# Kernel optimization log

Hardware: AMD Instinct MI355X
Metric: run time of the kernel (lower is better)

Reference implementation:

```python
import jax, jax.numpy as jnp
import numpy as np

IN_DIM = 1024
OUT_DIM = 2048
GRID = 5   # kan_config.grid_size
K = 3      # kan_config.spline_order


def b_splines(x, grid, k):
    """Cox-de Boor recursion.
    x: (N, D), grid: (D, G+2k+1) extended knots. Returns (N, D, G+k) basis values."""
    x = x[..., None]              # (N, D, 1)
    g = grid[None, :, :]          # (1, D, M)
    # degree-0 indicator bases
    B = ((x >= g[..., :-1]) & (x < g[..., 1:])).astype(x.dtype)  # (N, D, M-1)
    for p in range(1, k + 1):
        left = (x - g[..., : -(p + 1)]) / (g[..., p:-1] - g[..., : -(p + 1)])
        right = (g[..., p + 1:] - x) / (g[..., p + 1:] - g[..., 1:-p])
        B = left * B[..., :-1] + right * B[..., 1:]
    return B  # (N, D, G+k)


def setup_inputs() -> dict:
    key = jax.random.key(0)
    k1, k2, k3 = jax.random.split(key, 3)
    # inputs kept inside the spline grid range [-1, 1]
    x = jax.random.uniform(k1, (4, 2048, IN_DIM), jnp.float32, -1.0, 1.0)
    # uniform extended grid over [-1, 1] with k extra knots on each side
    h = 2.0 / GRID
    g = jnp.arange(-K, GRID + K + 1, dtype=jnp.float32) * h - 1.0  # (G+2K+1,)
    grid = jnp.broadcast_to(g, (IN_DIM, GRID + 2 * K + 1)).astype(jnp.float32)
    coef = (jax.random.normal(k2, (IN_DIM, OUT_DIM, GRID + K), jnp.float32) * 0.1)
    scale_base = jax.random.normal(k3, (IN_DIM, OUT_DIM), jnp.float32) * 0.1 + (1.0 / np.sqrt(IN_DIM)).astype(np.float32)
    scale_sp = jnp.ones((IN_DIM, OUT_DIM), jnp.float32)
    return {"x": x, "grid": grid, "coef": coef, "scale_base": scale_base, "scale_sp": scale_sp}


def reference(x, grid, coef, scale_base, scale_sp):
    shp = x.shape
    xf = x.reshape(-1, shp[-1])                 # (N, D)
    B = b_splines(xf, grid, K)                  # (N, D, G+K)
    coef_s = coef * scale_sp[:, :, None]        # fold per-edge spline scale into coefficients
    spline = jnp.einsum('ndg,dog->no', B, coef_s)          # (N, O)
    base = jnp.einsum('nd,do->no', jax.nn.silu(xf), scale_base)  # (N, O)
    out = base + spline
    return out.reshape(shp[:-1] + (OUT_DIM,))
```

## Files before the change

kernel.cpp:

```cpp
#include <hip/hip_runtime.h>
#include <hip/hip_bf16.h>
#include <cstdint>

typedef unsigned short u16;
typedef __bf16 bf16x8 __attribute__((ext_vector_type(8)));
typedef float  f32x4  __attribute__((ext_vector_type(4)));

typedef const __attribute__((address_space(1))) void* gptr_t;
typedef __attribute__((address_space(3))) void*       sptr_t;

#define IN_DIM  1024
#define OUT_DIM 2048
#define NROWS   8192
#define NB      8
#define KTOT    (IN_DIM * 9)
#define KSPL    (IN_DIM * 8)

#define WT_O 16
#define WT_D 64
#define TR_BLOCKS ((NROWS / 64) * (IN_DIM / 64))
#define WT_BLOCKS ((OUT_DIM / WT_O) * (IN_DIM / WT_D))

#define BK 32
#define TILE_U16 (256 * BK)
#define NKT (KTOT / BK)

__device__ __forceinline__ float rcp_fast(float v) { return __builtin_amdgcn_rcpf(v); }

__device__ __forceinline__ u16 f2b(float v) {
  uint32_t u = __float_as_uint(v);
  uint32_t r = (u + 0x7FFFu + ((u >> 16) & 1u)) >> 16;
  return (u16)r;
}

__device__ __forceinline__ uint32_t pkbf(float a, float b) {
  return (uint32_t)f2b(a) | ((uint32_t)f2b(b) << 16);
}

__device__ __forceinline__ uint4 basis_pack(float xval) {
  float tt = (xval + 1.0f) * 2.5f;
  float jf = floorf(tt);
  jf = fminf(fmaxf(jf, 0.0f), 4.0f);
  const float u = tt - jf;
  const int j = (int)jf;
  const float um = 1.0f - u;
  const float u2 = u * u, u3 = u2 * u;
  const float b0 = um * um * um * (1.0f / 6.0f);
  const float b1 = (3.0f * u3 - 6.0f * u2 + 4.0f) * (1.0f / 6.0f);
  const float b2 = (-3.0f * u3 + 3.0f * u2 + 3.0f * u + 1.0f) * (1.0f / 6.0f);
  const float b3 = u3 * (1.0f / 6.0f);
  const uint32_t e01 = pkbf(b0, b1), e23 = pkbf(b2, b3);
  const uint32_t o0 = e01 << 16;
  const uint32_t o12 = (e01 >> 16) | (e23 << 16);
  const uint32_t o3 = e23 >> 16;
  const int odd = j & 1, m = j >> 1;
  const uint32_t a0 = odd ? o0 : e01;
  const uint32_t a1 = odd ? o12 : e23;
  const uint32_t a2 = odd ? o3 : 0u;
  uint4 wv;
  wv.x = (m == 0) ? a0 : 0u;
  wv.y = (m == 1) ? a0 : ((m == 0) ? a1 : 0u);
  wv.z = (m == 2) ? a0 : ((m == 1) ? a1 : ((m == 0) ? a2 : 0u));
  wv.w = (m == 2) ? a1 : ((m == 1) ? a2 : 0u);
  return wv;
}

__global__ __launch_bounds__(256) void kan_prep(const float* __restrict__ x,
                                                const float* __restrict__ coef,
                                                const float* __restrict__ scale_base,
                                                const float* __restrict__ scale_sp,
                                                float* __restrict__ xT,
                                                u16* __restrict__ sil,
                                                u16* __restrict__ wt) {
  const int t = threadIdx.x;

  if (blockIdx.x < TR_BLOCKS) {
    __shared__ float tile[64][65];
    const int bi = blockIdx.x;
    const int n0 = (bi & 127) * 64;
    const int d0 = (bi >> 7) * 64;
    const int col = t & 63, rbase = t >> 6;
#pragma unroll
    for (int i = 0; i < 16; ++i) {
      const int r = rbase + i * 4;
      const float v = x[(size_t)(n0 + r) * IN_DIM + d0 + col];
      tile[r][col] = v;
      sil[(size_t)(n0 + r) * IN_DIM + d0 + col] =
          f2b(v * rcp_fast(1.0f + __expf(-v)));
    }
    __syncthreads();
#pragma unroll
    for (int i = 0; i < 16; ++i) {
      const int dd = rbase + i * 4;
      xT[(size_t)(d0 + dd) * NROWS + n0 + col] = tile[col][dd];
    }
  } else {
    __shared__ __align__(16) u16 tsp[WT_O][WT_D * 8 + 8];
    __shared__ __align__(16) u16 tsi[WT_O][WT_D + 8];
    const int bi = blockIdx.x - TR_BLOCKS;
    const int o0 = (bi % (OUT_DIM / WT_O)) * WT_O;
    const int d0 = (bi / (OUT_DIM / WT_O)) * WT_D;
    const int ol = t & (WT_O - 1), dl0 = t >> 4;
#pragma unroll
    for (int rep = 0; rep < WT_D / 16; ++rep) {
      const int dl = rep * 16 + dl0;
      const int d = d0 + dl, o = o0 + ol;
      const size_t doff = (size_t)d * OUT_DIM + o;
      const float ssp = scale_sp[doff];
      const float sbv = scale_base[doff];
      const float4* cp = (const float4*)(coef + doff * 8);
      float4 c0 = cp[0], c1 = cp[1];
      uint4 val;
      val.x = pkbf(c0.x * ssp, c0.y * ssp);
      val.y = pkbf(c0.z * ssp, c0.w * ssp);
      val.z = pkbf(c1.x * ssp, c1.y * ssp);
      val.w = pkbf(c1.z * ssp, c1.w * ssp);
      *(uint4*)&tsp[ol][dl * 8] = val;
      tsi[ol][dl] = f2b(sbv);
    }
    __syncthreads();
    for (int i = t; i < WT_O * 64; i += 256) {
      const int row = i >> 6, col = i & 63;
      *(uint4*)(wt + (size_t)(o0 + row) * KTOT + (size_t)(d0 + col) * 8) =
          *(const uint4*)&tsp[row][col * 8];
    }
    if (t < WT_O * 8) {
      const int row = t >> 3, col = t & 7;
      *(uint4*)(wt + (size_t)(o0 + row) * KTOT + KSPL + d0 + col * 8) =
          *(const uint4*)&tsi[row][col * 8];
    }
  }
}

__global__ __launch_bounds__(512, 2) void kan_gemm3(const float* __restrict__ xT,
                                                    const u16* __restrict__ sil,
                                                    const u16* __restrict__ Bt,
                                                    float* __restrict__ C) {
  __shared__ __align__(16) u16 As[4 * TILE_U16];
  __shared__ __align__(16) u16 Bs[4 * TILE_U16];
  const int tid  = threadIdx.x;
  const int lane = tid & 63;
  const int w    = tid >> 6;
  const int wm   = w >> 2, wn = w & 3;
  const int q    = lane >> 4, m16 = lane & 15;

  const int bid = (blockIdx.x & 7) * 32 + (blockIdx.x >> 3);
  const int gx = bid & 7;
  const int gy = bid >> 3;

  f32x4 acc[8][4];
#pragma unroll
  for (int i = 0; i < 8; ++i)
#pragma unroll
    for (int j = 0; j < 4; ++j) acc[i][j] = (f32x4){0.f, 0.f, 0.f, 0.f};

  const int rA  = lane >> 2;
  const int csw = ((lane & 3) ^ ((lane >> 3) & 3)) * 8;
  const u16* gB = Bt  + (size_t)(gx * 256 + w * 32 + rA) * KTOT + csw;
  const u16* sA = sil + (size_t)(gy * 256 + w * 32 + rA) * IN_DIM + csw;
  const int ldsw = w * 1024;

  const int arow = tid & 255;
  const int cd0  = tid >> 8;
  const int asw  = (arow >> 1) & 3;
  const int aw0  = arow * 32 + (cd0 ^ asw) * 8;
  const int aw1  = arow * 32 + ((cd0 + 2) ^ asw) * 8;
  const float* xp = xT + (size_t)cd0 * NROWS + gy * 256 + arow;

#define STAGE_B(T)                                                             \
  do {                                                                         \
    const int _bb = (T) & 3;                                                   \
    const size_t _k0 = (size_t)(T) * BK;                                       \
    __builtin_amdgcn_global_load_lds((gptr_t)(gB + _k0),                       \
        (sptr_t)&Bs[_bb * TILE_U16 + ldsw], 16, 0, 0);                         \
    __builtin_amdgcn_global_load_lds((gptr_t)(gB + (size_t)16 * KTOT + _k0),   \
        (sptr_t)&Bs[_bb * TILE_U16 + ldsw + 512], 16, 0, 0);                   \
  } while (0)

#define STAGE_A_SIL(T)                                                         \
  do {                                                                         \
    const int _ab = (T) & 3;                                                   \
    const size_t _db = (size_t)(T) * BK - KSPL;                                \
    __builtin_amdgcn_global_load_lds((gptr_t)(sA + _db),                       \
        (sptr_t)&As[_ab * TILE_U16 + ldsw], 16, 0, 0);                         \
    __builtin_amdgcn_global_load_lds((gptr_t)(sA + (size_t)16 * IN_DIM + _db), \
        (sptr_t)&As[_ab * TILE_U16 + ldsw + 512], 16, 0, 0);                   \
  } while (0)

#define WRITE_A_SPL(T, X0, X1)                                                 \
  do {                                                                         \
    const int _ab = (T) & 3;                                                   \
    *(uint4*)&As[_ab * TILE_U16 + aw0] = basis_pack(X0);                       \
    *(uint4*)&As[_ab * TILE_U16 + aw1] = basis_pack(X1);                       \
  } while (0)

  const int px8 = (q ^ ((m16 >> 1) & 3)) * 8;
  const int aoff = (wm * 128 + m16) * 32 + px8;
  const int boff = (wn * 64 + m16) * 32 + px8;

  bf16x8 fa[8], fb[4];

#define CORE(T)                                                                \
  do {                                                                         \
    const u16* _An = &As[(((T) + 1) & 3) * TILE_U16 + aoff];                   \
    const u16* _Bn = &Bs[(((T) + 1) & 3) * TILE_U16 + boff];                   \
    __builtin_amdgcn_s_setprio(1);                                             \
    _Pragma("unroll") for (int mt = 0; mt < 8; ++mt) {                         \
      _Pragma("unroll") for (int nt = 0; nt < 4; ++nt)                         \
        acc[mt][nt] = __builtin_amdgcn_mfma_f32_16x16x32_bf16(                 \
            fa[mt], fb[nt], acc[mt][nt], 0, 0, 0);                             \
      fa[mt] = *(const bf16x8*)&_An[mt * 512];                                 \
    }                                                                          \
    __builtin_amdgcn_s_setprio(0);                                             \
    _Pragma("unroll") for (int nt = 0; nt < 4; ++nt)                           \
      fb[nt] = *(const bf16x8*)&_Bn[nt * 512];                                 \
  } while (0)

#define ENDSYNC(VM)                                                            \
  do {                                                                         \
    asm volatile("s_waitcnt vmcnt(" #VM ")" ::: "memory");                     \
    asm volatile("s_waitcnt lgkmcnt(0)" ::: "memory");                         \
    __builtin_amdgcn_s_barrier();                                              \
  } while (0)

#define SP_REGION(T)                                                           \
  do {                                                                         \
    const float _x0 = xp[(size_t)(((T) + 2) * 4) * NROWS];                     \
    const float _x1 = xp[(size_t)(((T) + 2) * 4 + 2) * NROWS];                 \
    STAGE_B((T) + 3);                                                          \
    CORE(T);                                                                   \
    WRITE_A_SPL((T) + 2, _x0, _x1);                                            \
    ENDSYNC(2);                                                                \
  } while (0)

#define SI_REGION(T)                                                           \
  do {                                                                         \
    STAGE_A_SIL((T) + 2);                                                      \
    STAGE_B((T) + 3);                                                          \
    CORE(T);                                                                   \
    ENDSYNC(2);                                                                \
  } while (0)

  STAGE_B(0);
  STAGE_B(1);
  STAGE_B(2);
  {
    const float x00 = xp[0];
    const float x01 = xp[(size_t)2 * NROWS];
    const float x10 = xp[(size_t)4 * NROWS];
    const float x11 = xp[(size_t)6 * NROWS];
    WRITE_A_SPL(0, x00, x01);
    WRITE_A_SPL(1, x10, x11);
  }
  ENDSYNC(2);
  {
    const u16* _A0 = &As[aoff];
    const u16* _B0 = &Bs[boff];
#pragma unroll
    for (int nt = 0; nt < 4; ++nt) fb[nt] = *(const bf16x8*)&_B0[nt * 512];
#pragma unroll
    for (int mt = 0; mt < 8; ++mt) fa[mt] = *(const bf16x8*)&_A0[mt * 512];
  }

  for (int tb = 0; tb < 63; ++tb) {
#pragma unroll
    for (int j = 0; j < 4; ++j) {
      SP_REGION(tb * 4 + j);
    }
  }
  SP_REGION(252);
  SP_REGION(253);

  SI_REGION(254);
  SI_REGION(255);
  for (int tb = 0; tb < 7; ++tb) {
#pragma unroll
    for (int j = 0; j < 4; ++j) {
      SI_REGION(256 + tb * 4 + j);
    }
  }
  SI_REGION(284);

  STAGE_A_SIL(287);
  CORE(285);
  ENDSYNC(0);
  CORE(286);
  asm volatile("s_waitcnt lgkmcnt(0)" ::: "memory");
  __builtin_amdgcn_s_barrier();
  __builtin_amdgcn_s_setprio(1);
#pragma unroll
  for (int mt = 0; mt < 8; ++mt)
#pragma unroll
    for (int nt = 0; nt < 4; ++nt)
      acc[mt][nt] = __builtin_amdgcn_mfma_f32_16x16x32_bf16(fa[mt], fb[nt],
                                                            acc[mt][nt], 0, 0, 0);
  __builtin_amdgcn_s_setprio(0);

#undef SP_REGION
#undef SI_REGION
#undef ENDSYNC
#undef CORE
#undef WRITE_A_SPL
#undef STAGE_A_SIL
#undef STAGE_B

  const int row_base = gy * 256 + wm * 128 + q * 4;
  const int col_base = gx * 256 + wn * 64 + m16;
#pragma unroll
  for (int mt = 0; mt < 8; ++mt) {
#pragma unroll
    for (int nt = 0; nt < 4; ++nt) {
      const int r0 = row_base + mt * 16;
      const int c  = col_base + nt * 16;
#pragma unroll
      for (int r = 0; r < 4; ++r)
        C[(size_t)(r0 + r) * OUT_DIM + c] = acc[mt][nt][r];
    }
  }
}

__global__ __launch_bounds__(256) void kan_fallback(const float* __restrict__ x,
                                                    const float* __restrict__ grid,
                                                    const float* __restrict__ coef,
                                                    const float* __restrict__ scale_base,
                                                    const float* __restrict__ scale_sp,
                                                    float* __restrict__ out) {
  __shared__ float bs[IN_DIM * 9];
  const int n = blockIdx.x;
  const int t = threadIdx.x;
#pragma unroll
  for (int dd = 0; dd < IN_DIM / 256; ++dd) {
    const int d = t + dd * 256;
    const float xv = x[(size_t)n * IN_DIM + d];
    float tt = (xv + 1.0f) * 2.5f;
    float jf = floorf(tt);
    jf = fminf(fmaxf(jf, 0.0f), 4.0f);
    const float u = tt - jf;
    const int j = (int)jf;
    const float um = 1.0f - u;
    const float u2 = u * u, u3 = u2 * u;
    float* r = &bs[d * 9];
#pragma unroll
    for (int g = 0; g < NB; ++g) r[g] = 0.0f;
    r[j]     = um * um * um * (1.0f / 6.0f);
    r[j + 1] = (3.0f * u3 - 6.0f * u2 + 4.0f) * (1.0f / 6.0f);
    r[j + 2] = (-3.0f * u3 + 3.0f * u2 + 3.0f * u + 1.0f) * (1.0f / 6.0f);
    r[j + 3] = u3 * (1.0f / 6.0f);
    r[8]     = xv * rcp_fast(1.0f + __expf(-xv));
  }
  __syncthreads();
  const int o = blockIdx.y * 256 + t;
  float acc = 0.0f;
  for (int d = 0; d < IN_DIM; ++d) {
    const size_t doff = (size_t)d * OUT_DIM + o;
    const float4* cp = (const float4*)(coef + doff * 8);
    float4 c0 = cp[0], c1 = cp[1];
    const float* b = &bs[d * 9];
    float s = b[0] * c0.x + b[1] * c0.y + b[2] * c0.z + b[3] * c0.w +
              b[4] * c1.x + b[5] * c1.y + b[6] * c1.z + b[7] * c1.w;
    acc += s * scale_sp[doff] + b[8] * scale_base[doff];
  }
  out[(size_t)n * OUT_DIM + o] = acc;
}

extern "C" void kernel_launch(void* const* d_in, const int* in_sizes, int n_in,
                              void* d_out, int out_size, void* d_ws, size_t ws_size,
                              hipStream_t stream) {
  const float* x  = (const float*)d_in[0];
  const float* gr = (const float*)d_in[1];
  const float* cf = (const float*)d_in[2];
  const float* sb = (const float*)d_in[3];
  const float* sp = (const float*)d_in[4];
  float* out = (float*)d_out;

  const size_t xT_bytes  = (size_t)IN_DIM * NROWS * sizeof(float);
  const size_t sil_bytes = (size_t)NROWS * IN_DIM * sizeof(u16);
  const size_t wt_bytes  = (size_t)OUT_DIM * KTOT * sizeof(u16);
  const size_t need = xT_bytes + sil_bytes + wt_bytes;

  if (ws_size >= need) {
    float* xT = (float*)d_ws;
    u16* sil  = (u16*)((char*)d_ws + xT_bytes);
    u16* wt   = (u16*)((char*)d_ws + xT_bytes + sil_bytes);
    kan_prep<<<dim3(TR_BLOCKS + WT_BLOCKS), dim3(256), 0, stream>>>(
        x, cf, sb, sp, xT, sil, wt);
    kan_gemm3<<<dim3(256), dim3(512), 0, stream>>>(xT, sil, wt, out);
  } else {
    kan_fallback<<<dim3(NROWS, OUT_DIM / 256), dim3(256), 0, stream>>>(x, gr, cf, sb, sp, out);
  }
}
```

Baseline: 431.0 us.

## Fuse x transpose and SiLU into GEMM, reading x directly

Removes the transpose/SiLU blocks from the prep kernel and drops the xT and sil workspace buffers. The GEMM now reads x rows directly for the spline basis and computes SiLU in registers, writing bf16 into LDS instead of using async global-to-LDS loads. This cuts prep traffic (32MB xT write, 16MB sil write) but adds strided scalar x loads and SiLU arithmetic inside the GEMM main loop. Those extra loads may be poorly coalesced and can add VALU pressure.

```diff
diff --git a/kernel.cpp b/kernel.cpp
--- a/kernel.cpp
+++ b/kernel.cpp
@@ -18,7 +18,6 @@
 
 #define WT_O 16
 #define WT_D 64
-#define TR_BLOCKS ((NROWS / 64) * (IN_DIM / 64))
 #define WT_BLOCKS ((OUT_DIM / WT_O) * (IN_DIM / WT_D))
 
 #define BK 32
@@ -35,6 +34,10 @@
 
 __device__ __forceinline__ uint32_t pkbf(float a, float b) {
   return (uint32_t)f2b(a) | ((uint32_t)f2b(b) << 16);
+}
+
+__device__ __forceinline__ float silu_f(float v) {
+  return v * rcp_fast(1.0f + __expf(-v));
 }
 
 __device__ __forceinline__ uint4 basis_pack(float xval) {
@@ -65,75 +68,48 @@
   return wv;
 }
 
-__global__ __launch_bounds__(256) void kan_prep(const float* __restrict__ x,
-                                                const float* __restrict__ coef,
+__global__ __launch_bounds__(256) void kan_prep(const float* __restrict__ coef,
                                                 const float* __restrict__ scale_base,
                                                 const float* __restrict__ scale_sp,
-                                                float* __restrict__ xT,
-                                                u16* __restrict__ sil,
                                                 u16* __restrict__ wt) {
   const int t = threadIdx.x;
-
-  if (blockIdx.x < TR_BLOCKS) {
-    __shared__ float tile[64][65];
-    const int bi = blockIdx.x;
-    const int n0 = (bi & 127) * 64;
-    const int d0 = (bi >> 7) * 64;
-    const int col = t & 63, rbase = t >> 6;
-#pragma unroll
-    for (int i = 0; i < 16; ++i) {
-      const int r = rbase + i * 4;
-      const float v = x[(size_t)(n0 + r) * IN_DIM + d0 + col];
-      tile[r][col] = v;
-      sil[(size_t)(n0 + r) * IN_DIM + d0 + col] =
-          f2b(v * rcp_fast(1.0f + __expf(-v)));
-    }
-    __syncthreads();
-#pragma unroll
-    for (int i = 0; i < 16; ++i) {
-      const int dd = rbase + i * 4;
-      xT[(size_t)(d0 + dd) * NROWS + n0 + col] = tile[col][dd];
-    }
-  } else {
-    __shared__ __align__(16) u16 tsp[WT_O][WT_D * 8 + 8];
-    __shared__ __align__(16) u16 tsi[WT_O][WT_D + 8];
-    const int bi = blockIdx.x - TR_BLOCKS;
-    const int o0 = (bi % (OUT_DIM / WT_O)) * WT_O;
-    const int d0 = (bi / (OUT_DIM / WT_O)) * WT_D;
-    const int ol = t & (WT_O - 1), dl0 = t >> 4;
-#pragma unroll
-    for (int rep = 0; rep < WT_D / 16; ++rep) {
-      const int dl = rep * 16 + dl0;
-      const int d = d0 + dl, o = o0 + ol;
-      const size_t doff = (size_t)d * OUT_DIM + o;
-      const float ssp = scale_sp[doff];
-      const float sbv = scale_base[doff];
-      const float4* cp = (const float4*)(coef + doff * 8);
-      float4 c0 = cp[0], c1 = cp[1];
-      uint4 val;
-      val.x = pkbf(c0.x * ssp, c0.y * ssp);
-      val.y = pkbf(c0.z * ssp, c0.w * ssp);
-      val.z = pkbf(c1.x * ssp, c1.y * ssp);
-      val.w = pkbf(c1.z * ssp, c1.w * ssp);
-      *(uint4*)&tsp[ol][dl * 8] = val;
-      tsi[ol][dl] = f2b(sbv);
-    }
-    __syncthreads();
-    for (int i = t; i < WT_O * 64; i += 256) {
-      const int row = i >> 6, col = i & 63;
-      *(uint4*)(wt + (size_t)(o0 + row) * KTOT + (size_t)(d0 + col) * 8) =
-          *(const uint4*)&tsp[row][col * 8];
-    }
-    if (t < WT_O * 8) {
-      const int row = t >> 3, col = t & 7;
-      *(uint4*)(wt + (size_t)(o0 + row) * KTOT + KSPL + d0 + col * 8) =
-          *(const uint4*)&tsi[row][col * 8];
-    }
-  }
-}
-
-__global__ __launch_bounds__(512, 2) void kan_gemm3(const float* __restrict__ xT,
-                                                    const u16* __restrict__ sil,
+  __shared__ __align__(16) u16 tsp[WT_O][WT_D * 8 + 8];
+  __shared__ __align__(16) u16 tsi[WT_O][WT_D + 8];
+  const int bi = blockIdx.x;
+  const int o0 = (bi % (OUT_DIM / WT_O)) * WT_O;
+  const int d0 = (bi / (OUT_DIM / WT_O)) * WT_D;
+  const int ol = t & (WT_O - 1), dl0 = t >> 4;
+#pragma unroll
+  for (int rep = 0; rep < WT_D / 16; ++rep) {
+    const int dl = rep * 16 + dl0;
+    const int d = d0 + dl, o = o0 + ol;
+    const size_t doff = (size_t)d * OUT_DIM + o;
+    const float ssp = scale_sp[doff];
+    const float sbv = scale_base[doff];
+    const float4* cp = (const float4*)(coef + doff * 8);
+    float4 c0 = cp[0], c1 = cp[1];
+    uint4 val;
+    val.x = pkbf(c0.x * ssp, c0.y * ssp);
+    val.y = pkbf(c0.z * ssp, c0.w * ssp);
+    val.z = pkbf(c1.x * ssp, c1.y * ssp);
+    val.w = pkbf(c1.z * ssp, c1.w * ssp);
+    *(uint4*)&tsp[ol][dl * 8] = val;
+    tsi[ol][dl] = f2b(sbv);
+  }
+  __syncthreads();
+  for (int i = t; i < WT_O * 64; i += 256) {
+    const int row = i >> 6, col = i & 63;
+    *(uint4*)(wt + (size_t)(o0 + row) * KTOT + (size_t)(d0 + col) * 8) =
+        *(const uint4*)&tsp[row][col * 8];
+  }
+  if (t < WT_O * 8) {
+    const int row = t >> 3, col = t & 7;
+    *(uint4*)(wt + (size_t)(o0 + row) * KTOT + KSPL + d0 + col * 8) =
+        *(const uint4*)&tsi[row][col * 8];
+  }
+}
+
+__global__ __launch_bounds__(512, 2) void kan_gemm3(const float* __restrict__ x,
                                                     const u16* __restrict__ Bt,
                                                     float* __restrict__ C) {
   __shared__ __align__(16) u16 As[4 * TILE_U16];
@@ -156,8 +132,7 @@
 
   const int rA  = lane >> 2;
   const int csw = ((lane & 3) ^ ((lane >> 3) & 3)) * 8;
-  const u16* gB = Bt  + (size_t)(gx * 256 + w * 32 + rA) * KTOT + csw;
-  const u16* sA = sil + (size_t)(gy * 256 + w * 32 + rA) * IN_DIM + csw;
+  const u16* gB = Bt + (size_t)(gx * 256 + w * 32 + rA) * KTOT + csw;
   const int ldsw = w * 1024;
 
   const int arow = tid & 255;
@@ -165,7 +140,7 @@
   const int asw  = (arow >> 1) & 3;
   const int aw0  = arow * 32 + (cd0 ^ asw) * 8;
   const int aw1  = arow * 32 + ((cd0 + 2) ^ asw) * 8;
-  const float* xp = xT + (size_t)cd0 * NROWS + gy * 256 + arow;
+  const float* xrow = x + (size_t)(gy * 256 + arow) * IN_DIM;
 
 #define STAGE_B(T)                                                             \
   do {                                                                         \
@@ -177,21 +152,27 @@
         (sptr_t)&Bs[_bb * TILE_U16 + ldsw + 512], 16, 0, 0);                   \
   } while (0)
 
-#define STAGE_A_SIL(T)                                                         \
-  do {                                                                         \
-    const int _ab = (T) & 3;                                                   \
-    const size_t _db = (size_t)(T) * BK - KSPL;                                \
-    __builtin_amdgcn_global_load_lds((gptr_t)(sA + _db),                       \
-        (sptr_t)&As[_ab * TILE_U16 + ldsw], 16, 0, 0);                         \
-    __builtin_amdgcn_global_load_lds((gptr_t)(sA + (size_t)16 * IN_DIM + _db), \
-        (sptr_t)&As[_ab * TILE_U16 + ldsw + 512], 16, 0, 0);                   \
-  } while (0)
-
-#define WRITE_A_SPL(T, X0, X1)                                                 \
-  do {                                                                         \
-    const int _ab = (T) & 3;                                                   \
+#define WRITE_A_SPL(TS, X0, X1)                                                \
+  do {                                                                         \
+    const int _ab = (TS) & 3;                                                  \
     *(uint4*)&As[_ab * TILE_U16 + aw0] = basis_pack(X0);                       \
     *(uint4*)&As[_ab * TILE_U16 + aw1] = basis_pack(X1);                       \
+  } while (0)
+
+#define WRITE_A_SIL(TS, XA, XB, XC, XD)                                        \
+  do {                                                                         \
+    const int _ab = (TS) & 3;                                                  \
+    uint4 _w0, _w1;                                                            \
+    _w0.x = pkbf(silu_f(XA.x), silu_f(XA.y));                                  \
+    _w0.y = pkbf(silu_f(XA.z), silu_f(XA.w));                                  \
+    _w0.z = pkbf(silu_f(XB.x), silu_f(XB.y));                                  \
+    _w0.w = pkbf(silu_f(XB.z), silu_f(XB.w));                                  \
+    _w1.x = pkbf(silu_f(XC.x), silu_f(XC.y));                                  \
+    _w1.y = pkbf(silu_f(XC.z), silu_f(XC.w));                                  \
+    _w1.z = pkbf(silu_f(XD.x), silu_f(XD.y));                                  \
+    _w1.w = pkbf(silu_f(XD.z), silu_f(XD.w));                                  \
+    *(uint4*)&As[_ab * TILE_U16 + aw0] = _w0;                                  \
+    *(uint4*)&As[_ab * TILE_U16 + aw1] = _w1;                                  \
   } while (0)
 
   const int px8 = (q ^ ((m16 >> 1) & 3)) * 8;
@@ -225,8 +206,8 @@
 
 #define SP_REGION(T)                                                           \
   do {                                                                         \
-    const float _x0 = xp[(size_t)(((T) + 2) * 4) * NROWS];                     \
-    const float _x1 = xp[(size_t)(((T) + 2) * 4 + 2) * NROWS];                 \
+    const float _x0 = xrow[((T) + 2) * 4 + cd0];                               \
+    const float _x1 = xrow[((T) + 2) * 4 + cd0 + 2];                           \
     STAGE_B((T) + 3);                                                          \
     CORE(T);                                                                   \
     WRITE_A_SPL((T) + 2, _x0, _x1);                                            \
@@ -235,20 +216,25 @@
 
 #define SI_REGION(T)                                                           \
   do {                                                                         \
-    STAGE_A_SIL((T) + 2);                                                      \
+    const float* _xp = xrow + ((T) + 2 - 256) * 32 + cd0 * 8;                  \
+    const float4 _xa = *(const float4*)(_xp);                                  \
+    const float4 _xb = *(const float4*)(_xp + 4);                              \
+    const float4 _xc = *(const float4*)(_xp + 16);                             \
+    const float4 _xd = *(const float4*)(_xp + 20);                             \
     STAGE_B((T) + 3);                                                          \
     CORE(T);                                                                   \
+    WRITE_A_SIL((T) + 2, _xa, _xb, _xc, _xd);                                  \
     ENDSYNC(2);                                                                \
   } while (0)
 
-  STAGE_B(0);
-  STAGE_B(1);
-  STAGE_B(2);
   {
-    const float x00 = xp[0];
-    const float x01 = xp[(size_t)2 * NROWS];
-    const float x10 = xp[(size_t)4 * NROWS];
-    const float x11 = xp[(size_t)6 * NROWS];
+    const float x00 = xrow[cd0];
+    const float x01 = xrow[cd0 + 2];
+    const float x10 = xrow[4 + cd0];
+    const float x11 = xrow[4 + cd0 + 2];
+    STAGE_B(0);
+    STAGE_B(1);
+    STAGE_B(2);
     WRITE_A_SPL(0, x00, x01);
     WRITE_A_SPL(1, x10, x11);
   }
@@ -281,9 +267,16 @@
   }
   SI_REGION(284);
 
-  STAGE_A_SIL(287);
-  CORE(285);
-  ENDSYNC(0);
+  {
+    const float* _xp = xrow + (287 - 256) * 32 + cd0 * 8;
+    const float4 _xa = *(const float4*)(_xp);
+    const float4 _xb = *(const float4*)(_xp + 4);
+    const float4 _xc = *(const float4*)(_xp + 16);
+    const float4 _xd = *(const float4*)(_xp + 20);
+    CORE(285);
+    WRITE_A_SIL(287, _xa, _xb, _xc, _xd);
+    ENDSYNC(0);
+  }
   CORE(286);
   asm volatile("s_waitcnt lgkmcnt(0)" ::: "memory");
   __builtin_amdgcn_s_barrier();
@@ -300,8 +293,8 @@
 #undef SI_REGION
 #undef ENDSYNC
 #undef CORE
+#undef WRITE_A_SIL
 #undef WRITE_A_SPL
-#undef STAGE_A_SIL
 #undef STAGE_B
 
   const int row_base = gy * 256 + wm * 128 + q * 4;
@@ -373,18 +366,12 @@
   const float* sp = (const float*)d_in[4];
   float* out = (float*)d_out;
 
-  const size_t xT_bytes  = (size_t)IN_DIM * NROWS * sizeof(float);
-  const size_t sil_bytes = (size_t)NROWS * IN_DIM * sizeof(u16);
-  const size_t wt_bytes  = (size_t)OUT_DIM * KTOT * sizeof(u16);
-  const size_t need = xT_bytes + sil_bytes + wt_bytes;
-
-  if (ws_size >= need) {
-    float* xT = (float*)d_ws;
-    u16* sil  = (u16*)((char*)d_ws + xT_bytes);
-    u16* wt   = (u16*)((char*)d_ws + xT_bytes + sil_bytes);
-    kan_prep<<<dim3(TR_BLOCKS + WT_BLOCKS), dim3(256), 0, stream>>>(
-        x, cf, sb, sp, xT, sil, wt);
-    kan_gemm3<<<dim3(256), dim3(512), 0, stream>>>(xT, sil, wt, out);
+  const size_t wt_bytes = (size_t)OUT_DIM * KTOT * sizeof(u16);
+
+  if (ws_size >= wt_bytes) {
+    u16* wt = (u16*)d_ws;
+    kan_prep<<<dim3(WT_BLOCKS), dim3(256), 0, stream>>>(cf, sb, sp, wt);
+    kan_gemm3<<<dim3(256), dim3(512), 0, stream>>>(x, wt, out);
   } else {
     kan_fallback<<<dim3(NROWS, OUT_DIM / 256), dim3(256), 0, stream>>>(x, gr, cf, sb, sp, out);
   }
```

After: 539.8 us. 1.25x slower.
